# Optimization experiments

Measured on AMD Instinct MI355X. Metric: run time of the kernel, lower is better.

Reference implementation:

```python
import jax, jax.numpy as jnp
import numpy as np

B, S, QD = 4, 2048, 1024
NH, KVH, DH = 16, 4, 64
WIN = 256  # sliding_window


def setup_inputs() -> dict:
    key = jax.random.key(0)
    ks = jax.random.split(key, 5)
    s = QD ** -0.5
    return {
        "hidden_states": jax.random.normal(ks[0], (B, S, QD), jnp.float32),
        "Wq": jax.random.normal(ks[1], (QD, NH * DH), jnp.float32) * s,
        "Wk": jax.random.normal(ks[2], (QD, KVH * DH), jnp.float32) * s,
        "Wv": jax.random.normal(ks[3], (QD, KVH * DH), jnp.float32) * s,
        "Wo": jax.random.normal(ks[4], (NH * DH, QD), jnp.float32) * s,
    }


def reference(hidden_states, Wq, Wk, Wv, Wo):
    x = hidden_states
    # QKV projections (torch Linear, no bias)
    q = (x @ Wq).reshape(B, S, NH, DH).transpose(0, 2, 1, 3)    # [B,NH,S,DH]
    k = (x @ Wk).reshape(B, S, KVH, DH).transpose(0, 2, 1, 3)   # [B,KVH,S,DH]
    v = (x @ Wv).reshape(B, S, KVH, DH).transpose(0, 2, 1, 3)
    # GQA: instead of repeat_interleave on k/v, group query heads per kv head
    g = NH // KVH
    qg = q.reshape(B, KVH, g, S, DH)
    scale = DH ** -0.5
    scores = jnp.einsum('bkgsd,bktd->bkgst', qg, k) * scale      # [B,KVH,g,S,S]
    # Sliding-window mask: torch SDPA treats a FLOAT mask as ADDITIVE, and the
    # original builds a 0/1 float mask (1 where |i-j| <= window). Faithful: add it.
    idx = jnp.arange(S)
    win = (jnp.abs(idx[:, None] - idx[None, :]) <= WIN).astype(scores.dtype)  # [S,S]
    scores = scores + win  # broadcast over B,KVH,g (same mask for all batch/heads)
    attn = jax.nn.softmax(scores, axis=-1)
    out = jnp.einsum('bkgst,bktd->bkgsd', attn, v)               # [B,KVH,g,S,DH]
    out = out.reshape(B, NH, S, DH).transpose(0, 2, 1, 3).reshape(B, S, NH * DH)
    return out @ Wo
```

## Files before the change

### kernel.cpp

```cpp
#include <hip/hip_runtime.h>
#include <hip/hip_bf16.h>


using short8 = __attribute__((ext_vector_type(8))) short;
using f32x4  = __attribute__((ext_vector_type(4))) float;
using f32x16 = __attribute__((ext_vector_type(16))) float;
using uint2v = __attribute__((ext_vector_type(2))) unsigned int;

#define GLDS(g, l) __builtin_amdgcn_global_load_lds( \
    (const __attribute__((address_space(1))) void*)(g), \
    (__attribute__((address_space(3))) void*)(l), 16, 0, 0)

__device__ __forceinline__ unsigned short f2bf(float f) {
  union { float f; unsigned u; } v; v.f = f;
  unsigned r = v.u + 0x7fffu + ((v.u >> 16) & 1u);
  return (unsigned short)(r >> 16);
}

__device__ __forceinline__ unsigned cvtpk(float lo, float hi) {
  unsigned r;
  asm("v_cvt_pk_bf16_f32 %0, %1, %2" : "=v"(r) : "v"(lo), "v"(hi));
  return r;
}

__global__ __launch_bounds__(256) void wtr_kernel(
    const float* __restrict__ Wq, const float* __restrict__ Wk,
    const float* __restrict__ Wv, const float* __restrict__ Wo,
    unsigned short* __restrict__ WqkvT, unsigned short* __restrict__ WoT)
{
  __shared__ float tile[32][33];
  const int bx = blockIdx.x;
  const int by = blockIdx.y;
  const float* src; unsigned short* dst; int C, ct;
  if (by < 32)      { src = Wq; dst = WqkvT;               C = 1024; ct = by; }
  else if (by < 40) { src = Wk; dst = WqkvT + 1024 * 1024; C = 256;  ct = by - 32; }
  else if (by < 48) { src = Wv; dst = WqkvT + 1280 * 1024; C = 256;  ct = by - 40; }
  else              { src = Wo; dst = WoT;                 C = 1024; ct = by - 48; }
  const int tx = threadIdx.x & 31, ty = threadIdx.x >> 5;
  const int c0 = ct * 32, r0 = bx * 32;
#pragma unroll
  for (int i = 0; i < 4; ++i)
    tile[ty + i * 8][tx] = src[(size_t)(r0 + ty + i * 8) * C + c0 + tx];
  __syncthreads();
#pragma unroll
  for (int i = 0; i < 4; ++i) {
    int c = ty + i * 8;
    dst[(size_t)(c0 + c) * 1024 + r0 + tx] = f2bf(tile[tx][c]);
  }
}

__global__ __launch_bounds__(256) void qkv_gemm_kernel(
    const float* __restrict__ X, const unsigned short* __restrict__ Bt,
    unsigned short* __restrict__ Qo, unsigned short* __restrict__ Ko,
    unsigned short* __restrict__ Vto)
{
  __shared__ __align__(16) unsigned short As[128 * 32];
  __shared__ __align__(16) unsigned short Bs[128 * 32];
  const int m0 = blockIdx.x * 128;
  const int n0 = blockIdx.y * 128;
  const int t = threadIdx.x;
  const int w = t >> 6, l = t & 63;
  const int wr = w >> 1, wc = w & 1;

  f32x4 acc[4][4] = {};

  const size_t aoff = (size_t)(m0 + w * 16 + (l >> 2)) * 1024 + (size_t)((l & 3) * 8);
  const size_t boff = (size_t)(n0 + w * 16 + (l >> 2)) * 1024 + (size_t)((l & 3) * 8);
  unsigned short* Aw0 = &As[w * 512 + l * 8];
  unsigned short* Aw1 = &As[(w + 4) * 512 + l * 8];
  const bool qk = (n0 < 1280);

  for (int kt = 0; kt < 1024; kt += 32) {
    GLDS(Bt + boff + kt,             &Bs[w * 512]);
    GLDS(Bt + boff + 64 * 1024 + kt, &Bs[(w + 4) * 512]);
    float4 fa0 = *reinterpret_cast<const float4*>(X + aoff + kt);
    float4 fa1 = *reinterpret_cast<const float4*>(X + aoff + kt + 4);
    float4 fb0 = *reinterpret_cast<const float4*>(X + aoff + 64 * 1024 + kt);
    float4 fb1 = *reinterpret_cast<const float4*>(X + aoff + 64 * 1024 + kt + 4);
    uint4 ua, ub;
    ua.x = cvtpk(fa0.x, fa0.y); ua.y = cvtpk(fa0.z, fa0.w);
    ua.z = cvtpk(fa1.x, fa1.y); ua.w = cvtpk(fa1.z, fa1.w);
    ub.x = cvtpk(fb0.x, fb0.y); ub.y = cvtpk(fb0.z, fb0.w);
    ub.z = cvtpk(fb1.x, fb1.y); ub.w = cvtpk(fb1.z, fb1.w);
    *reinterpret_cast<uint4*>(Aw0) = ua;
    *reinterpret_cast<uint4*>(Aw1) = ub;
    __syncthreads();

    short8 af[4], bfr[4];
#pragma unroll
    for (int mi = 0; mi < 4; ++mi) {
      int row = wr * 64 + mi * 16 + (l & 15);
      af[mi] = *reinterpret_cast<const short8*>(&As[row * 32 + (l >> 4) * 8]);
    }
#pragma unroll
    for (int ni = 0; ni < 4; ++ni) {
      int row = wc * 64 + ni * 16 + (l & 15);
      bfr[ni] = *reinterpret_cast<const short8*>(&Bs[row * 32 + (l >> 4) * 8]);
    }
    if (qk) {
#pragma unroll
      for (int mi = 0; mi < 4; ++mi)
#pragma unroll
        for (int ni = 0; ni < 4; ++ni)
          acc[mi][ni] = __builtin_amdgcn_mfma_f32_16x16x32_bf16(bfr[ni], af[mi], acc[mi][ni], 0, 0, 0);
    } else {
#pragma unroll
      for (int mi = 0; mi < 4; ++mi)
#pragma unroll
        for (int ni = 0; ni < 4; ++ni)
          acc[mi][ni] = __builtin_amdgcn_mfma_f32_16x16x32_bf16(af[mi], bfr[ni], acc[mi][ni], 0, 0, 0);
    }
    __syncthreads();
  }

  const int lo = (l >> 4) * 4;

  if (qk) {
#pragma unroll
    for (int mi = 0; mi < 4; ++mi) {
      const int tok = m0 + wr * 64 + mi * 16 + (l & 15);
      const int bb = tok >> 11, ss = tok & 2047;
      const int T5 = ss >> 5, q5 = ss & 31;
#pragma unroll
      for (int ni = 0; ni < 4; ++ni) {
        const int ddb = n0 + wc * 64 + ni * 16;
        uint2 wv;
        wv.x = cvtpk(acc[mi][ni][0], acc[mi][ni][1]);
        wv.y = cvtpk(acc[mi][ni][2], acc[mi][ni][3]);
        size_t base; unsigned short* dstp;
        if (ddb < 1024) {
          int hh = ddb >> 6, kk = (ddb >> 4) & 3;
          base = ((((size_t)(bb * 16 + hh)) * 64 + T5) * 4 + kk) * 512; dstp = Qo;
        } else {
          int kvh = (ddb - 1024) >> 6, kk = (ddb >> 4) & 3;
          base = ((((size_t)(bb * 4 + kvh)) * 64 + T5) * 4 + kk) * 512; dstp = Ko;
        }
        *reinterpret_cast<uint2*>(dstp + base + (lo >> 3) * 256 + q5 * 8 + (lo & 7)) = wv;
      }
    }
  } else {
#pragma unroll
    for (int ni = 0; ni < 4; ++ni) {
      const int dd = n0 + wc * 64 + ni * 16 + (l & 15);
      const int kvh = (dd - 1280) >> 6, d6 = dd & 63;
#pragma unroll
      for (int mi = 0; mi < 4; ++mi) {
        const int tokb = m0 + wr * 64 + mi * 16 + lo;
        const int bb = tokb >> 11, ss = tokb & 2047;
        const int T5 = ss >> 5;
        const int f = (d6 >> 5) * 2 + (mi & 1);
        uint2 wv;
        wv.x = cvtpk(acc[mi][ni][0], acc[mi][ni][1]);
        wv.y = cvtpk(acc[mi][ni][2], acc[mi][ni][3]);
        size_t base = ((((size_t)(bb * 4 + kvh)) * 64 + T5) * 4 + f) * 512;
        *reinterpret_cast<uint2*>(Vto + base + ((lo >> 3) & 1) * 256 + (d6 & 31) * 8 + (lo & 7)) = wv;
      }
    }
  }
}

__global__ __launch_bounds__(256) void outproj_gemm_kernel(
    const unsigned short* __restrict__ A, const unsigned short* __restrict__ Bt,
    float* __restrict__ Co)
{
  __shared__ __align__(16) unsigned short As[128 * 32];
  __shared__ __align__(16) unsigned short Bs[128 * 32];
  const int m0 = blockIdx.x * 128;
  const int n0 = blockIdx.y * 128;
  const int t = threadIdx.x;
  const int w = t >> 6, l = t & 63;
  const int wr = w >> 1, wc = w & 1;

  f32x4 acc[4][4] = {};

  const size_t aoff = (size_t)(m0 + w * 16 + (l >> 2)) * 1024 + (size_t)((l & 3) * 8);
  const size_t boff = (size_t)(n0 + w * 16 + (l >> 2)) * 1024 + (size_t)((l & 3) * 8);

  for (int kt = 0; kt < 1024; kt += 32) {
    GLDS(A  + aoff + kt,             &As[w * 512]);
    GLDS(A  + aoff + 64 * 1024 + kt, &As[(w + 4) * 512]);
    GLDS(Bt + boff + kt,             &Bs[w * 512]);
    GLDS(Bt + boff + 64 * 1024 + kt, &Bs[(w + 4) * 512]);
    __syncthreads();

    short8 af[4], bfr[4];
#pragma unroll
    for (int mi = 0; mi < 4; ++mi) {
      int row = wr * 64 + mi * 16 + (l & 15);
      af[mi] = *reinterpret_cast<const short8*>(&As[row * 32 + (l >> 4) * 8]);
    }
#pragma unroll
    for (int ni = 0; ni < 4; ++ni) {
      int row = wc * 64 + ni * 16 + (l & 15);
      bfr[ni] = *reinterpret_cast<const short8*>(&Bs[row * 32 + (l >> 4) * 8]);
    }
#pragma unroll
    for (int mi = 0; mi < 4; ++mi)
#pragma unroll
      for (int ni = 0; ni < 4; ++ni)
        acc[mi][ni] = __builtin_amdgcn_mfma_f32_16x16x32_bf16(af[mi], bfr[ni], acc[mi][ni], 0, 0, 0);
    __syncthreads();
  }

#pragma unroll
  for (int mi = 0; mi < 4; ++mi)
#pragma unroll
    for (int ni = 0; ni < 4; ++ni)
#pragma unroll
      for (int r = 0; r < 4; ++r) {
        int m = m0 + wr * 64 + mi * 16 + (l >> 4) * 4 + r;
        int n = n0 + wc * 64 + ni * 16 + (l & 15);
        Co[((size_t)m << 10) + n] = acc[mi][ni][r];
      }
}

__global__ __launch_bounds__(256, 4) void attn_kernel(
    const unsigned short* __restrict__ Qf, const unsigned short* __restrict__ Kf,
    const unsigned short* __restrict__ Vf, unsigned short* __restrict__ AO)
{
  const int t = threadIdx.x, w = t >> 6, l = t & 63;
  const int hi = l >> 5, ln = l & 31;

  const int orig = blockIdx.x;
  const int swz = (orig & 7) * 128 + (orig >> 3);
  const int hf = swz >> 4;
  const int qt = swz & 15;
  const int b = hf >> 4, h = hf & 15, kvh = h >> 2;
  const int q0 = qt * 128 + w * 32;
  const int qrow = q0 + ln;

  const unsigned short* Qp = Qf + (((size_t)hf * 64 + qt * 4 + w) * 4) * 512;
  const unsigned short* Kt = Kf + ((size_t)(b * 4 + kvh) * 256) * 512 + l * 8;
  const unsigned short* Vt = Vf + ((size_t)(b * 4 + kvh) * 256) * 512 + l * 8;

  short8 qf[4];
#pragma unroll
  for (int kk = 0; kk < 4; ++kk)
    qf[kk] = *reinterpret_cast<const short8*>(Qp + kk * 512 + l * 8);

  f32x16 oA = {}, oB = {};
  float lsum = 0.f;
  const float C1  = 0.125f * 1.44269504f;
  const float L2E = 1.44269504f;
  const float FM  = 12.0f;

  for (int T = 0; T < 64; ++T) {
    short8 kf0 = *reinterpret_cast<const short8*>(Kt);
    short8 kf1 = *reinterpret_cast<const short8*>(Kt + 512);
    short8 kf2 = *reinterpret_cast<const short8*>(Kt + 1024);
    short8 kf3 = *reinterpret_cast<const short8*>(Kt + 1536);
    f32x16 s = {};
    s = __builtin_amdgcn_mfma_f32_32x32x16_bf16(kf0, qf[0], s, 0, 0, 0);
    s = __builtin_amdgcn_mfma_f32_32x32x16_bf16(kf1, qf[1], s, 0, 0, 0);
    s = __builtin_amdgcn_mfma_f32_32x32x16_bf16(kf2, qf[2], s, 0, 0, 0);
    s = __builtin_amdgcn_mfma_f32_32x32x16_bf16(kf3, qf[3], s, 0, 0, 0);
    short8 vf0 = *reinterpret_cast<const short8*>(Vt);
    short8 vf1 = *reinterpret_cast<const short8*>(Vt + 512);
    short8 vf2 = *reinterpret_cast<const short8*>(Vt + 1024);
    short8 vf3 = *reinterpret_cast<const short8*>(Vt + 1536);
    Kt += 2048; Vt += 2048;

    const int kv0 = T * 32;
    const int d = q0 - kv0;
    float p[16];
    if (d == 256 || d == -256) {
      const int qmb = qrow - kv0 - 4 * hi;
#pragma unroll
      for (int r = 0; r < 16; ++r) {
        const int kc = (r & 3) + 8 * (r >> 2);
        int df = qmb - kc; df = df < 0 ? -df : df;
        p[r] = __builtin_amdgcn_exp2f(
            __builtin_fmaf(s[r], C1, (df <= 256 ? L2E : 0.f) - FM));
      }
    } else {
      const float cc = ((d <= 224 && d >= -224) ? L2E : 0.f) - FM;
#pragma unroll
      for (int i = 0; i < 16; ++i)
        p[i] = __builtin_amdgcn_exp2f(__builtin_fmaf(s[i], C1, cc));
    }

    float s8[8], s4[4];
#pragma unroll
    for (int i = 0; i < 8; ++i) s8[i] = p[i] + p[i + 8];
#pragma unroll
    for (int i = 0; i < 4; ++i) s4[i] = s8[i] + s8[i + 4];
    float sum = (s4[0] + s4[1]) + (s4[2] + s4[3]);
    {
      uint2v sw = __builtin_amdgcn_permlane32_swap(__float_as_uint(sum), __float_as_uint(sum), false, false);
      sum = __uint_as_float(sw[0]) + __uint_as_float(sw[1]);
    }
    lsum += sum;

#pragma unroll
    for (int ks = 0; ks < 2; ++ks) {
      unsigned a0 = cvtpk(p[ks * 8 + 0], p[ks * 8 + 1]);
      unsigned a1 = cvtpk(p[ks * 8 + 2], p[ks * 8 + 3]);
      unsigned b0 = cvtpk(p[ks * 8 + 4], p[ks * 8 + 5]);
      unsigned b1 = cvtpk(p[ks * 8 + 6], p[ks * 8 + 7]);
      uint2v s0 = __builtin_amdgcn_permlane32_swap(a0, b0, false, false);
      uint2v s1 = __builtin_amdgcn_permlane32_swap(a1, b1, false, false);
      union { unsigned u[4]; short8 v; } pf;
      pf.u[0] = s0[0]; pf.u[1] = s1[0]; pf.u[2] = s0[1]; pf.u[3] = s1[1];
      oA = __builtin_amdgcn_mfma_f32_32x32x16_bf16(ks ? vf1 : vf0, pf.v, oA, 0, 0, 0);
      oB = __builtin_amdgcn_mfma_f32_32x32x16_bf16(ks ? vf3 : vf2, pf.v, oB, 0, 0, 0);
    }
  }

  const float inv = 1.f / lsum;
  unsigned short* Op = AO + ((size_t)(b * 2048 + qrow)) * 1024 + h * 64;
#pragma unroll
  for (int qd = 0; qd < 4; ++qd) {
    uint2 wv;
    wv.x = cvtpk(oA[4 * qd + 0] * inv, oA[4 * qd + 1] * inv);
    wv.y = cvtpk(oA[4 * qd + 2] * inv, oA[4 * qd + 3] * inv);
    *reinterpret_cast<uint2*>(Op + qd * 8 + hi * 4) = wv;
  }
#pragma unroll
  for (int qd = 0; qd < 4; ++qd) {
    uint2 wv;
    wv.x = cvtpk(oB[4 * qd + 0] * inv, oB[4 * qd + 1] * inv);
    wv.y = cvtpk(oB[4 * qd + 2] * inv, oB[4 * qd + 3] * inv);
    *reinterpret_cast<uint2*>(Op + 32 + qd * 8 + hi * 4) = wv;
  }
}

extern "C" void kernel_launch(void* const* d_in, const int* in_sizes, int n_in,
                              void* d_out, int out_size, void* d_ws, size_t ws_size,
                              hipStream_t stream)
{
  const float* X  = (const float*)d_in[0];
  const float* Wq = (const float*)d_in[1];
  const float* Wk = (const float*)d_in[2];
  const float* Wv = (const float*)d_in[3];
  const float* Wo = (const float*)d_in[4];
  float* out = (float*)d_out;
  char* ws = (char*)d_ws;

  unsigned short* WqkvT = (unsigned short*)(ws);
  unsigned short* WoT   = (unsigned short*)(ws + 3145728);
  unsigned short* Q     = (unsigned short*)(ws + 5242880);
  unsigned short* Kc    = (unsigned short*)(ws + 22020096);
  unsigned short* Vt    = (unsigned short*)(ws + 26214400);
  unsigned short* AO    = (unsigned short*)(ws + 30408704);

  wtr_kernel<<<dim3(32, 80), 256, 0, stream>>>(Wq, Wk, Wv, Wo, WqkvT, WoT);
  qkv_gemm_kernel<<<dim3(64, 12), 256, 0, stream>>>(X, WqkvT, Q, Kc, Vt);
  attn_kernel<<<1024, 256, 0, stream>>>(Q, Kc, Vt, AO);
  outproj_gemm_kernel<<<dim3(64, 8), 256, 0, stream>>>(AO, WoT, out);
}
```

Baseline: 198.5 us.

## Software-pipeline QK^T of next KV tile ahead of softmax and PV

Restructures the attention inner loop into a two-stage software pipeline: the QK^T MFMAs for tile T+1 are issued before the softmax and PV accumulation of tile T, using ping-pong score registers. The aim is to overlap matrix-core work with the exp/convert VALU work and the latency of the K/V global loads. It raises register pressure because two score accumulators are live at once, which could lower occupancy.

After: 242.7 us. +22.2%, slower.

```diff
diff --git a/kernel.cpp b/kernel.cpp
--- a/kernel.cpp
+++ b/kernel.cpp
@@ -244,25 +244,9 @@
   const float L2E = 1.44269504f;
   const float FM  = 12.0f;
 
-  for (int T = 0; T < 64; ++T) {
-    short8 kf0 = *reinterpret_cast<const short8*>(Kt);
-    short8 kf1 = *reinterpret_cast<const short8*>(Kt + 512);
-    short8 kf2 = *reinterpret_cast<const short8*>(Kt + 1024);
-    short8 kf3 = *reinterpret_cast<const short8*>(Kt + 1536);
-    f32x16 s = {};
-    s = __builtin_amdgcn_mfma_f32_32x32x16_bf16(kf0, qf[0], s, 0, 0, 0);
-    s = __builtin_amdgcn_mfma_f32_32x32x16_bf16(kf1, qf[1], s, 0, 0, 0);
-    s = __builtin_amdgcn_mfma_f32_32x32x16_bf16(kf2, qf[2], s, 0, 0, 0);
-    s = __builtin_amdgcn_mfma_f32_32x32x16_bf16(kf3, qf[3], s, 0, 0, 0);
-    short8 vf0 = *reinterpret_cast<const short8*>(Vt);
-    short8 vf1 = *reinterpret_cast<const short8*>(Vt + 512);
-    short8 vf2 = *reinterpret_cast<const short8*>(Vt + 1024);
-    short8 vf3 = *reinterpret_cast<const short8*>(Vt + 1536);
-    Kt += 2048; Vt += 2048;
-
-    const int kv0 = T * 32;
+  auto softmax_p = [&](const f32x16& s, int Tt, float (&p)[16]) {
+    const int kv0 = Tt * 32;
     const int d = q0 - kv0;
-    float p[16];
     if (d == 256 || d == -256) {
       const int qmb = qrow - kv0 - 4 * hi;
 #pragma unroll
@@ -278,19 +262,21 @@
       for (int i = 0; i < 16; ++i)
         p[i] = __builtin_amdgcn_exp2f(__builtin_fmaf(s[i], C1, cc));
     }
-
     float s8[8], s4[4];
 #pragma unroll
     for (int i = 0; i < 8; ++i) s8[i] = p[i] + p[i + 8];
 #pragma unroll
     for (int i = 0; i < 4; ++i) s4[i] = s8[i] + s8[i + 4];
     float sum = (s4[0] + s4[1]) + (s4[2] + s4[3]);
-    {
-      uint2v sw = __builtin_amdgcn_permlane32_swap(__float_as_uint(sum), __float_as_uint(sum), false, false);
-      sum = __uint_as_float(sw[0]) + __uint_as_float(sw[1]);
-    }
-    lsum += sum;
-
+    uint2v sw = __builtin_amdgcn_permlane32_swap(__float_as_uint(sum), __float_as_uint(sum), false, false);
+    lsum += __uint_as_float(sw[0]) + __uint_as_float(sw[1]);
+  };
+
+  auto pv_accum = [&](const float (&p)[16], const unsigned short* Vb) {
+    short8 vf0 = *reinterpret_cast<const short8*>(Vb);
+    short8 vf1 = *reinterpret_cast<const short8*>(Vb + 512);
+    short8 vf2 = *reinterpret_cast<const short8*>(Vb + 1024);
+    short8 vf3 = *reinterpret_cast<const short8*>(Vb + 1536);
 #pragma unroll
     for (int ks = 0; ks < 2; ++ks) {
       unsigned a0 = cvtpk(p[ks * 8 + 0], p[ks * 8 + 1]);
@@ -304,6 +290,49 @@
       oA = __builtin_amdgcn_mfma_f32_32x32x16_bf16(ks ? vf1 : vf0, pf.v, oA, 0, 0, 0);
       oB = __builtin_amdgcn_mfma_f32_32x32x16_bf16(ks ? vf3 : vf2, pf.v, oB, 0, 0, 0);
     }
+  };
+
+  auto qk = [&](const unsigned short* Kb) -> f32x16 {
+    short8 kf0 = *reinterpret_cast<const short8*>(Kb);
+    short8 kf1 = *reinterpret_cast<const short8*>(Kb + 512);
+    short8 kf2 = *reinterpret_cast<const short8*>(Kb + 1024);
+    short8 kf3 = *reinterpret_cast<const short8*>(Kb + 1536);
+    f32x16 s = {};
+    s = __builtin_amdgcn_mfma_f32_32x32x16_bf16(kf0, qf[0], s, 0, 0, 0);
+    s = __builtin_amdgcn_mfma_f32_32x32x16_bf16(kf1, qf[1], s, 0, 0, 0);
+    s = __builtin_amdgcn_mfma_f32_32x32x16_bf16(kf2, qf[2], s, 0, 0, 0);
+    s = __builtin_amdgcn_mfma_f32_32x32x16_bf16(kf3, qf[3], s, 0, 0, 0);
+    return s;
+  };
+
+  f32x16 sA = qk(Kt);
+  f32x16 sB;
+
+  for (int T = 0; T < 62; T += 2) {
+    sB = qk(Kt + 2048);
+    {
+      float pA[16];
+      softmax_p(sA, T, pA);
+      pv_accum(pA, Vt);
+    }
+    sA = qk(Kt + 4096);
+    {
+      float pB[16];
+      softmax_p(sB, T + 1, pB);
+      pv_accum(pB, Vt + 2048);
+    }
+    Kt += 4096; Vt += 4096;
+  }
+  sB = qk(Kt + 2048);
+  {
+    float pA[16];
+    softmax_p(sA, 62, pA);
+    pv_accum(pA, Vt);
+  }
+  {
+    float pB[16];
+    softmax_p(sB, 63, pB);
+    pv_accum(pB, Vt + 2048);
   }
 
   const float inv = 1.f / lsum;
```
